# Kernel optimization log

Hardware: AMD Instinct MI355X
Metric: run time of the kernel (lower is better)

The kernel has to match this reference:

```python
import jax, jax.numpy as jnp
import numpy as np

B, N, DIM = 8, 2048, 1024
EPSILON = 0.03
SCALE = 1.0 / np.sqrt(DIM).astype(np.float32)


def setup_inputs() -> dict:
    key = jax.random.key(0)
    ks = jax.random.split(key, 5)
    Q = jax.random.normal(ks[0], (B, N, DIM), dtype=jnp.float32)
    K = jax.random.normal(ks[1], (B, N, DIM), dtype=jnp.float32)
    V = jax.random.normal(ks[2], (B, N, DIM), dtype=jnp.float32)
    # H_net: Linear(dim, dim//2) -> SiLU -> Linear(dim//2, 1); init like torch default scale-ish
    W1 = jax.random.normal(ks[3], (DIM, DIM // 2), dtype=jnp.float32) * (1.0 / np.sqrt(DIM))
    b1 = jnp.zeros((DIM // 2,), dtype=jnp.float32)
    W2 = jax.random.normal(ks[4], (DIM // 2, 1), dtype=jnp.float32) * (1.0 / np.sqrt(DIM // 2))
    b2 = jnp.zeros((1,), dtype=jnp.float32)
    return {"Q": Q, "K": K, "V": V, "W1": W1, "b1": b1, "W2": W2, "b2": b2}


def _mlp(x, W1, b1, W2, b2):
    h = jax.nn.silu(x @ W1 + b1)  # [B,N,dim//2]
    return h @ W2 + b2            # [B,N,1]


def reference(Q, K, V, W1, b1, W2, b2):
    def energy(q, v):
        # scores [B,N,N]
        A = jax.nn.softmax(jnp.einsum('bnd,bmd->bnm', q, K) * SCALE, axis=-1)
        attn_out = jnp.einsum('bnm,bmd->bnd', A, v)
        H = jnp.sum(_mlp(attn_out, W1, b1, W2, b2))
        return H, attn_out

    # grads of scalar energy H w.r.t. Q and V (dH_dV is computed per the
    # original code but discarded by the final split; only dH_dQ survives)
    (dH_dQ, dH_dV), attn_out = jax.grad(energy, argnums=(0, 1), has_aux=True)(Q, V)
    # S_new = cat([Q,V]) + eps*cat([dH_dV, -dH_dQ]); split -> V_new = V - eps*dH_dQ
    V_new = V - EPSILON * dH_dQ
    return V_new + attn_out
```

## Files before the change

### kernel.cpp

```cpp
#include <hip/hip_runtime.h>

typedef __bf16 bf16;
typedef long i64;
typedef __attribute__((ext_vector_type(8))) __bf16 bf16x8;
typedef __attribute__((ext_vector_type(4))) float f32x4;
typedef __attribute__((ext_vector_type(4))) int i32x4;

#define MEMFENCE asm volatile("" ::: "memory")

__device__ __forceinline__ unsigned char tofp8(float x) {
    return (unsigned char)(__builtin_amdgcn_cvt_pk_fp8_f32(x, x, 0, false) & 0xff);
}

__device__ __forceinline__ void gload16(const void* g, void* l) {
    __builtin_amdgcn_global_load_lds(
        (const __attribute__((address_space(1))) void*)g,
        (__attribute__((address_space(3))) void*)l,
        16, 0, 0);
}

template<int EPI, int F8>
__global__ __launch_bounds__(512, 1)
void gemm8p(const void* __restrict__ A, const void* __restrict__ Bm,
            void* __restrict__ Cp, int Kdim, int lda, int ldb, int ldc,
            long sA, long sB, long sC, float alpha,
            const float* __restrict__ aux1, const bf16* __restrict__ aux3)
{
    constexpr int ES = F8 ? 1 : 2;
    __shared__ __align__(16) char smem[163840];

    const int gx = gridDim.x, gy = gridDim.y;
    int lin = blockIdx.x + gx * (blockIdx.y + gy * blockIdx.z);
    const int q = (gx * gy * gridDim.z) >> 3;
    lin = (lin & 7) * q + (lin >> 3);
    const int bx = lin % gx;
    const int rem0 = lin / gx;
    const int by = rem0 % gy;
    const int bz = rem0 / gy;

    const int t0 = threadIdx.x;
    const int w = t0 >> 6, lane = t0 & 63;
    const int wm = w >> 2, wn = w & 3;
    const int m0 = by * 256, n0 = bx * 256;
    const long zb = bz;

    const char* Ab = (const char*)A + ((size_t)zb * sA + (size_t)m0 * lda) * ES;
    const char* Bb = (const char*)Bm + ((size_t)zb * sB + (size_t)n0 * ldb) * ES;

    const int sr16 = lane >> 2;
    const int sceB = F8 ? ((((lane & 3) ^ (sr16 & 3) ^ (((lane >> 5) & 1) << 1)) << 4))
                        : ((((lane & 3) << 4) ^ (((lane >> 5) & 1) << 5)));
    const int r0s = (w >> 1) * 16 + sr16;
    const int c0sB = (w & 1) * 64 + sceB;
    const char* gA0 = Ab + (size_t)r0s * lda * ES + c0sB;
    const char* gA1 = Ab + (size_t)(128 + r0s) * lda * ES + c0sB;
    const char* gB0 = Bb + (size_t)r0s * ldb * ES + c0sB;
    const char* gB1 = Bb + (size_t)(128 + r0s) * ldb * ES + c0sB;
    const size_t a64 = (size_t)64 * lda * ES, b64 = (size_t)64 * ldb * ES;
    const int ldsW0 = w * 1024, ldsW1 = (8 + w) * 1024;

    const int lr = lane & 15, lkq = lane >> 4;
    const int phx = ((lane >> 3) & 1) << 5;
    const int frag_base = F8 ? (lr * 64) : ((lr * 64 + lkq * 16) ^ phx);
    const int e0 = (((0 + (lkq >> 1)) ^ (lr & 3) ^ (((lr >> 3) & 1) << 1)) << 4) + ((lkq & 1) << 3);
    const int e1 = (((2 + (lkq >> 1)) ^ (lr & 3) ^ (((lr >> 3) & 1) << 1)) << 4) + ((lkq & 1) << 3);
    const char* aR = smem + wm * 16384 + frag_base;
    const char* bR = smem + 98304 + (wn >> 1) * 16384 + (wn & 1) * 8192 + frag_base;

    f32x4 acc[8][4] = {};
    const int NTt = Kdim >> (F8 ? 7 : 6);

    auto stgA = [&](int h, int u, int off) {
        char* L = smem + off + h * 16384;
        const char* g = h ? gA1 : gA0;
        gload16(g + (size_t)u * 128,        L + ldsW0);
        gload16(g + a64 + (size_t)u * 128,  L + ldsW1);
    };
    auto stgB = [&](int h, int u, int p) {
        char* L = smem + 98304 + p * 32768 + h * 16384;
        const char* g = h ? gB1 : gB0;
        gload16(g + (size_t)u * 128,        L + ldsW0);
        gload16(g + b64 + (size_t)u * 128,  L + ldsW1);
    };

    stgA(0, 0, 0);     stgA(1, 0, 0);     stgB(0, 0, 0); stgB(1, 0, 0);
    stgA(0, 1, 32768); stgA(1, 1, 32768); stgB(0, 1, 1); stgB(1, 1, 1);
    asm volatile("s_waitcnt vmcnt(8)" ::: "memory");
    __builtin_amdgcn_s_barrier();
    MEMFENCE;

    bf16x8 a[4][2], bl[2][2], bh[2][2];
    i64 a8[4][2][2], bl8[2][2][2], bh8[2][2][2];

#define RD8(DST, BASE, SUB)                                                \
    DST[0] = *(const i64*)((BASE) + (SUB) * 1024 + e0);                    \
    DST[1] = *(const i64*)((BASE) + (SUB) * 1024 + e1);

    if constexpr (!F8) {
        #pragma unroll
        for (int mf = 0; mf < 4; ++mf)
            #pragma unroll
            for (int ks = 0; ks < 2; ++ks)
                a[mf][ks] = *(const bf16x8*)(aR + (mf * 2 + ks) * 1024);
        #pragma unroll
        for (int nf = 0; nf < 2; ++nf)
            #pragma unroll
            for (int ks = 0; ks < 2; ++ks)
                bh[nf][ks] = *(const bf16x8*)(bR + ((2 + nf) * 2 + ks) * 1024);
    } else {
        #pragma unroll
        for (int mf = 0; mf < 4; ++mf)
            #pragma unroll
            for (int ks = 0; ks < 2; ++ks) { RD8(a8[mf][ks], aR, mf * 2 + ks) }
        #pragma unroll
        for (int nf = 0; nf < 2; ++nf)
            #pragma unroll
            for (int ks = 0; ks < 2; ++ks) { RD8(bh8[nf][ks], bR, (2 + nf) * 2 + ks) }
    }

#define QUADQ(MFB, NFB, AARR, BARR)                                                     \
    __builtin_amdgcn_s_setprio(1);                                                      \
    _Pragma("unroll")                                                                   \
    for (int ks = 0; ks < 2; ++ks)                                                      \
        _Pragma("unroll")                                                               \
        for (int mf = 0; mf < 4; ++mf)                                                  \
            _Pragma("unroll")                                                           \
            for (int nf = 0; nf < 2; ++nf)                                              \
                acc[(MFB) + mf][(NFB) + nf] = __builtin_amdgcn_mfma_f32_16x16x32_bf16(  \
                    AARR[mf][ks], BARR[nf][ks], acc[(MFB) + mf][(NFB) + nf], 0, 0, 0);  \
    __builtin_amdgcn_s_setprio(0);

#define QUAD8(MFB, NFB, AARR, BARR)                                                     \
    __builtin_amdgcn_s_setprio(1);                                                      \
    _Pragma("unroll")                                                                   \
    for (int ks = 0; ks < 2; ++ks)                                                      \
        _Pragma("unroll")                                                               \
        for (int k2 = 0; k2 < 2; ++k2)                                                  \
            _Pragma("unroll")                                                           \
            for (int mf = 0; mf < 4; ++mf)                                              \
                _Pragma("unroll")                                                       \
                for (int nf = 0; nf < 2; ++nf)                                          \
                    acc[(MFB) + mf][(NFB) + nf] =                                       \
                        __builtin_amdgcn_mfma_f32_16x16x32_fp8_fp8(                     \
                            AARR[mf][ks][k2], BARR[nf][ks][k2],                         \
                            acc[(MFB) + mf][(NFB) + nf], 0, 0, 0);                      \
    __builtin_amdgcn_s_setprio(0);

    int aOff = 0, aOff1 = 32768, sOff = 65536;
    for (int u = 0; u < NTt; ++u) {
        const int p = u & 1;
        const char* aP  = aR + aOff;
        const char* aP1 = aR + aOff1;
        const char* bP  = bR + p * 32768;
        const char* bP1 = bR + (p ^ 1) * 32768;
        const bool st2 = (u + 2 < NTt), nx = (u + 1 < NTt);

        if (st2) stgA(0, u + 2, sOff);
        if constexpr (!F8) {
            #pragma unroll
            for (int nf = 0; nf < 2; ++nf)
                #pragma unroll
                for (int ks = 0; ks < 2; ++ks)
                    bl[nf][ks] = *(const bf16x8*)(bP + (nf * 2 + ks) * 1024);
            QUADQ(0, 2, a, bh)
        } else {
            #pragma unroll
            for (int nf = 0; nf < 2; ++nf)
                #pragma unroll
                for (int ks = 0; ks < 2; ++ks) { RD8(bl8[nf][ks], bP, nf * 2 + ks) }
            QUAD8(0, 2, a8, bh8)
        }

        if (st2) stgA(1, u + 2, sOff);
        if constexpr (!F8) {
            QUADQ(0, 0, a, bl)
            #pragma unroll
            for (int mf = 0; mf < 4; ++mf)
                #pragma unroll
                for (int ks = 0; ks < 2; ++ks)
                    a[mf][ks] = *(const bf16x8*)(aP + ((4 + mf) * 2 + ks) * 1024);
        } else {
            QUAD8(0, 0, a8, bl8)
            #pragma unroll
            for (int mf = 0; mf < 4; ++mf)
                #pragma unroll
                for (int ks = 0; ks < 2; ++ks) { RD8(a8[mf][ks], aP, (4 + mf) * 2 + ks) }
        }
        MEMFENCE;
        if (st2)     asm volatile("s_waitcnt vmcnt(4)" ::: "memory");
        else if (nx) asm volatile("s_waitcnt vmcnt(0)" ::: "memory");
        __builtin_amdgcn_s_barrier();
        MEMFENCE;

        if (st2) stgB(0, u + 2, p);
        if constexpr (!F8) { QUADQ(4, 0, a, bl) } else { QUAD8(4, 0, a8, bl8) }

        if (st2) stgB(1, u + 2, p);
        if constexpr (!F8) {
            QUADQ(4, 2, a, bh)
            if (nx) {
                #pragma unroll
                for (int mf = 0; mf < 4; ++mf)
                    #pragma unroll
                    for (int ks = 0; ks < 2; ++ks)
                        a[mf][ks] = *(const bf16x8*)(aP1 + (mf * 2 + ks) * 1024);
                #pragma unroll
                for (int nf = 0; nf < 2; ++nf)
                    #pragma unroll
                    for (int ks = 0; ks < 2; ++ks)
                        bh[nf][ks] = *(const bf16x8*)(bP1 + ((2 + nf) * 2 + ks) * 1024);
            }
        } else {
            QUAD8(4, 2, a8, bh8)
            if (nx) {
                #pragma unroll
                for (int mf = 0; mf < 4; ++mf)
                    #pragma unroll
                    for (int ks = 0; ks < 2; ++ks) { RD8(a8[mf][ks], aP1, mf * 2 + ks) }
                #pragma unroll
                for (int nf = 0; nf < 2; ++nf)
                    #pragma unroll
                    for (int ks = 0; ks < 2; ++ks) { RD8(bh8[nf][ks], bP1, (2 + nf) * 2 + ks) }
            }
        }
        MEMFENCE;
        __builtin_amdgcn_s_barrier();
        MEMFENCE;

        const int tmp = aOff; aOff = aOff1; aOff1 = sOff; sOff = tmp;
    }
#undef QUADQ
#undef QUAD8
#undef RD8

    const int rb  = m0 + wm * 128 + lkq * 4;
    const int cb0 = n0 + wn * 64 + lr;
    #pragma unroll
    for (int mf = 0; mf < 8; ++mf) {
        #pragma unroll
        for (int r = 0; r < 4; ++r) {
            const int rw = rb + mf * 16 + r;
            float rd = 0.f;
            if (EPI == 1) {
                const size_t gr = zb * 2048 + rw;
                rd = aux1[gr] + aux1[16384 + gr] + aux1[32768 + gr] + aux1[49152 + gr];
            }
            #pragma unroll
            for (int nf = 0; nf < 4; ++nf) {
                const int c = cb0 + nf * 16;
                const size_t ix = (size_t)rw * ldc + c;
                const float v = acc[mf][nf][r];
                if (EPI == 0) {
                    ((bf16*)Cp + zb * sC)[ix] = (bf16)(alpha * v);
                } else if (EPI == 1) {
                    const bf16* Am = aux3 + zb * sC;
                    const float t = (float)Am[ix] * (v * alpha - rd) * 64.f;
                    ((unsigned char*)Cp + zb * sC)[ix] = tofp8(t);
                } else {
                    float* C = (float*)Cp + zb * sC;
                    const float* Vv = aux1 + zb * sC;
                    const bf16* AOv = aux3 + zb * sC;
                    C[ix] = Vv[ix] + (float)AOv[ix] - alpha * v;
                }
            }
        }
    }
}

template<int EPI, int NF>
__global__ __launch_bounds__(512, 1)
void gemm_nc(const bf16* __restrict__ A, const bf16* __restrict__ Bm,
             void* __restrict__ Cp, int Kdim, int lda, int ldb, int ldc,
             long sA, long sB, long sC, float alpha,
             const float* __restrict__ aux1, const float* __restrict__ aux2,
             float* __restrict__ rds)
{
    constexpr int SB = NF * 4096;
    __shared__ __align__(16) char smem[65536 + 4 * SB];

    const int gx = gridDim.x, gy = gridDim.y;
    int lin = blockIdx.x + gx * (blockIdx.y + gy * blockIdx.z);
    const int q = (gx * gy * gridDim.z) >> 3;
    lin = (lin & 7) * q + (lin >> 3);
    const int bx = lin % gx;
    const int rem0 = lin / gx;
    const int by = rem0 % gy;
    const int bz = rem0 / gy;

    const int t0 = threadIdx.x;
    const int w = t0 >> 6, lane = t0 & 63;
    const int wm = w >> 2, wn = w & 3;
    const int m0 = by * 256, n0 = bx * (64 * NF);
    const long zb = bz;

    const bf16* Ab = A  + zb * sA + (size_t)m0 * lda;
    const bf16* Bb = Bm + zb * sB + (size_t)n0 * ldb;

    const int sr16 = lane >> 2;
    const int sce  = ((((lane & 3) << 4) ^ (((lane >> 5) & 1) << 5))) >> 1;
    const int stg0 = w * 2, stg1 = w * 2 + 1;
    const bf16* pA0 = Ab + (size_t)(stg0 * 16 + sr16) * lda + sce;
    const bf16* pA1 = Ab + (size_t)(stg1 * 16 + sr16) * lda + sce;
    const bf16* pB0 = Bb + (size_t)((NF == 4 ? stg0 : w) * 16 + sr16) * ldb + sce;
    const bf16* pB1 = Bb + (size_t)(stg1 * 16 + sr16) * ldb + sce;

    const int lr = lane & 15, lkq = lane >> 4;
    const int phx = ((lane >> 3) & 1) << 5;
    const int frag_base = lr * 64 + lkq * 16;

    f32x4 acc[8][NF] = {};
    const int NT = Kdim >> 5;

    auto issueSlot = [&](int p) {
        char* lA = smem + (p & 3) * 16384;
        char* lB = smem + 65536 + (p & 3) * SB;
        const int kt = p << 5;
        gload16(pA0 + kt, lA + stg0 * 1024);
        gload16(pA1 + kt, lA + stg1 * 1024);
        if (NF == 4) {
            gload16(pB0 + kt, lB + stg0 * 1024);
            gload16(pB1 + kt, lB + stg1 * 1024);
        } else {
            gload16(pB0 + kt, lB + w * 1024);
        }
    };
    auto rdA = [&](const char* base, int sub) {
        return *(const bf16x8*)(base + (((sub << 10) + frag_base) ^ phx));
    };

    issueSlot(0); issueSlot(1); issueSlot(2);
    if (NF == 4) asm volatile("s_waitcnt vmcnt(4)" ::: "memory");
    else         asm volatile("s_waitcnt vmcnt(3)" ::: "memory");
    __builtin_amdgcn_s_barrier();
    MEMFENCE;

    bf16x8 alo[4], ahi[4], b0[NF], b1[NF];
    {
        const char* cA = smem;
        const char* cB = smem + 65536;
        #pragma unroll
        for (int mf = 0; mf < 4; ++mf) alo[mf] = rdA(cA, wm * 8 + mf);
        #pragma unroll
        for (int nf = 0; nf < NF; ++nf) b0[nf] = rdA(cB, wn * NF + nf);
    }

    auto stepBody = [&](int SL, int s, bf16x8 (&bA)[NF], bf16x8 (&bB)[NF]) {
        if (s + 3 < NT) issueSlot(s + 3);
        const char* cA = smem + SL * 16384;
        #pragma unroll
        for (int mf = 0; mf < 4; ++mf) ahi[mf] = rdA(cA, wm * 8 + 4 + mf);

        __builtin_amdgcn_s_setprio(1);
        #pragma unroll
        for (int mf = 0; mf < 4; ++mf)
            #pragma unroll
            for (int nf = 0; nf < NF; ++nf)
                acc[mf][nf] = __builtin_amdgcn_mfma_f32_16x16x32_bf16(alo[mf], bA[nf], acc[mf][nf], 0, 0, 0);
        __builtin_amdgcn_s_setprio(0);

        if (s + 1 < NT) {
            const int NS = (SL + 1) & 3;
            const char* nA = smem + NS * 16384;
            const char* nB = smem + 65536 + NS * SB;
            #pragma unroll
            for (int mf = 0; mf < 4; ++mf) alo[mf] = rdA(nA, wm * 8 + mf);
            #pragma unroll
            for (int nf = 0; nf < NF; ++nf) bB[nf] = rdA(nB, wn * NF + nf);
        }

        __builtin_amdgcn_s_setprio(1);
        #pragma unroll
        for (int mf = 0; mf < 4; ++mf)
            #pragma unroll
            for (int nf = 0; nf < NF; ++nf)
                acc[4 + mf][nf] = __builtin_amdgcn_mfma_f32_16x16x32_bf16(ahi[mf], bA[nf], acc[4 + mf][nf], 0, 0, 0);
        __builtin_amdgcn_s_setprio(0);

        MEMFENCE;
        if (s + 3 < NT) {
            if (NF == 4) asm volatile("s_waitcnt vmcnt(4)" ::: "memory");
            else         asm volatile("s_waitcnt vmcnt(3)" ::: "memory");
        } else {
            asm volatile("s_waitcnt vmcnt(0)" ::: "memory");
        }
        __builtin_amdgcn_s_barrier();
        MEMFENCE;
    };

    for (int s = 0; s < NT; s += 2) {
        stepBody(s & 3, s, b0, b1);
        stepBody((s + 1) & 3, s + 1, b1, b0);
    }

    const int rb  = m0 + wm * 128 + lkq * 4;
    const int cb0 = n0 + wn * (NF * 16) + lr;

    if (EPI == 0 || EPI == 4) {
        #pragma unroll
        for (int mf = 0; mf < 8; ++mf)
            #pragma unroll
            for (int nf = 0; nf < NF; ++nf) {
                const int c = cb0 + nf * 16;
                #pragma unroll
                for (int r = 0; r < 4; ++r) {
                    const int rw = rb + mf * 16 + r;
                    const size_t ix = (size_t)rw * ldc + c;
                    if (EPI == 0)
                        ((bf16*)Cp + zb * sC)[ix] = (bf16)(alpha * acc[mf][nf][r]);
                    else
                        ((unsigned char*)Cp + zb * sC)[ix] = tofp8(alpha * acc[mf][nf][r]);
                }
            }
    } else {
        float* smemF = (float*)smem;
        #pragma unroll
        for (int mf = 0; mf < 8; ++mf) {
            #pragma unroll
            for (int r = 0; r < 4; ++r) {
                const int rw = rb + mf * 16 + r;
                float pd = 0.f;
                #pragma unroll
                for (int nf = 0; nf < NF; ++nf) {
                    const int c = cb0 + nf * 16;
                    const float v = acc[mf][nf][r];
                    const float u = v + aux1[c];
                    const float sg = 1.f / (1.f + __expf(-u));
                    const float dd = sg * (1.f + u * (1.f - sg));
                    const float uval = dd * aux2[c];
                    ((unsigned char*)Cp)[(size_t)rw * ldc + c] = tofp8(uval * 16.f);
                    pd += uval * v;
                }
                #pragma unroll
                for (int o = 1; o < 16; o <<= 1) pd += __shfl_xor(pd, o, 64);
                if (lr == 0)
                    smemF[wn * 256 + wm * 128 + mf * 16 + lkq * 4 + r] = pd;
            }
        }
        __syncthreads();
        if (t0 < 256) {
            const float s4 = smemF[t0] + smemF[256 + t0] + smemF[512 + t0] + smemF[768 + t0];
            rds[(size_t)bx * 16384 + m0 + t0] = s4;
        }
    }
}

template<bool DN, int TM>
__device__ __forceinline__ void transcast_body(
                 const float* __restrict__ in, bf16* __restrict__ outN,
                 void* __restrict__ outT, int R, int C, int bx, int by, int bz,
                 float (*ts)[65])
{
    const int t = threadIdx.x;
    const int c0 = bx * 64, r0 = by * 64;
    const size_t zoff = (size_t)bz * R * C;

    const int rr = t >> 2, cc = (t & 3) * 16;
    float4 f[4];
    const float* src = in + zoff + (size_t)(r0 + rr) * C + c0 + cc;
    #pragma unroll
    for (int i = 0; i < 4; ++i) f[i] = *(const float4*)(src + 4 * i);

    if (DN) {
        bf16x8 h0, h1;
        #pragma unroll
        for (int i = 0; i < 2; ++i) {
            h0[i*4+0] = (bf16)f[i].x;   h0[i*4+1] = (bf16)f[i].y;
            h0[i*4+2] = (bf16)f[i].z;   h0[i*4+3] = (bf16)f[i].w;
            h1[i*4+0] = (bf16)f[i+2].x; h1[i*4+1] = (bf16)f[i+2].y;
            h1[i*4+2] = (bf16)f[i+2].z; h1[i*4+3] = (bf16)f[i+2].w;
        }
        bf16* dst = outN + zoff + (size_t)(r0 + rr) * C + c0 + cc;
        *(bf16x8*)dst = h0;
        *(bf16x8*)(dst + 8) = h1;
    }
    if (TM) {
        #pragma unroll
        for (int i = 0; i < 4; ++i) {
            ts[rr][cc + 4*i + 0] = f[i].x;
            ts[rr][cc + 4*i + 1] = f[i].y;
            ts[rr][cc + 4*i + 2] = f[i].z;
            ts[rr][cc + 4*i + 3] = f[i].w;
        }
        __syncthreads();
        const int ct = t >> 2, rr4 = (t & 3) * 16;
        if (TM == 1) {
            bf16x8 o0, o1;
            #pragma unroll
            for (int i = 0; i < 8; ++i) o0[i] = (bf16)ts[rr4 + i][ct];
            #pragma unroll
            for (int i = 0; i < 8; ++i) o1[i] = (bf16)ts[rr4 + 8 + i][ct];
            bf16* dst = (bf16*)outT + zoff + (size_t)(c0 + ct) * R + r0 + rr4;
            *(bf16x8*)dst = o0;
            *(bf16x8*)(dst + 8) = o1;
        } else {
            i32x4 o;
            #pragma unroll
            for (int g = 0; g < 4; ++g) {
                int v = __builtin_amdgcn_cvt_pk_fp8_f32(ts[rr4 + 4*g + 0][ct], ts[rr4 + 4*g + 1][ct], 0, false);
                v = __builtin_amdgcn_cvt_pk_fp8_f32(ts[rr4 + 4*g + 2][ct], ts[rr4 + 4*g + 3][ct], v, true);
                o[g] = v;
            }
            unsigned char* dst = (unsigned char*)outT + zoff + (size_t)(c0 + ct) * R + r0 + rr4;
            *(i32x4*)dst = o;
        }
    }
}

__global__ __launch_bounds__(256)
void trans_all(const float* __restrict__ Q, const float* __restrict__ Km,
               const float* __restrict__ V, const float* __restrict__ W1,
               bf16* __restrict__ Qb, bf16* __restrict__ Kb, unsigned char* __restrict__ KbT8,
               bf16* __restrict__ Vb, bf16* __restrict__ VbT, bf16* __restrict__ W1T)
{
    __shared__ float ts[64][65];
    const int z = blockIdx.z;
    if (z < 8) {
        transcast_body<true, 0>(Q, Qb, nullptr, 2048, 1024, blockIdx.x, blockIdx.y, z, ts);
    } else if (z < 16) {
        transcast_body<true, 2>(Km, Kb, KbT8, 2048, 1024, blockIdx.x, blockIdx.y, z - 8, ts);
    } else if (z < 24) {
        transcast_body<true, 1>(V, Vb, VbT, 2048, 1024, blockIdx.x, blockIdx.y, z - 16, ts);
    } else {
        if (blockIdx.x < 8 && blockIdx.y < 16)
            transcast_body<false, 1>(W1, nullptr, W1T, 1024, 512, blockIdx.x, blockIdx.y, 0, ts);
    }
}

__global__ __launch_bounds__(256)
void softmax_k(const bf16* __restrict__ S, bf16* __restrict__ A)
{
    const size_t row = blockIdx.x;
    const int t = threadIdx.x;
    const int wid = t >> 6, lane = t & 63;
    __shared__ float r1[4], r2[4];

    bf16x8 v = *(const bf16x8*)(S + row * 2048 + t * 8);
    float f[8];
    float mx = -1e30f;
    #pragma unroll
    for (int i = 0; i < 8; ++i) { f[i] = (float)v[i]; mx = fmaxf(mx, f[i]); }
    #pragma unroll
    for (int o = 32; o; o >>= 1) mx = fmaxf(mx, __shfl_xor(mx, o, 64));
    if (!lane) r1[wid] = mx;
    __syncthreads();
    mx = fmaxf(fmaxf(r1[0], r1[1]), fmaxf(r1[2], r1[3]));

    float sum = 0.f;
    #pragma unroll
    for (int i = 0; i < 8; ++i) { f[i] = __expf(f[i] - mx); sum += f[i]; }
    #pragma unroll
    for (int o = 32; o; o >>= 1) sum += __shfl_xor(sum, o, 64);
    if (!lane) r2[wid] = sum;
    __syncthreads();
    sum = r2[0] + r2[1] + r2[2] + r2[3];

    const float inv = 1.f / sum;
    bf16x8 ov;
    #pragma unroll
    for (int i = 0; i < 8; ++i) ov[i] = (bf16)(f[i] * inv);
    *(bf16x8*)(A + row * 2048 + t * 8) = ov;
}

extern "C" void kernel_launch(void* const* d_in, const int* in_sizes, int n_in,
                              void* d_out, int out_size, void* d_ws, size_t ws_size,
                              hipStream_t stream)
{
    const float* Q  = (const float*)d_in[0];
    const float* Km = (const float*)d_in[1];
    const float* V  = (const float*)d_in[2];
    const float* W1 = (const float*)d_in[3];
    const float* b1 = (const float*)d_in[4];
    const float* W2 = (const float*)d_in[5];
    float* out = (float*)d_out;

    char* ws = (char*)d_ws;
    bf16* Amat = (bf16*)(ws);
    bf16* AO   = (bf16*)(ws + 67108864);
    bf16* Kb   = AO;
    unsigned char* KbT8 = (unsigned char*)(ws + 100663296);
    float* rdSlab = (float*)(ws + 117440512);
    bf16* Vb   = (bf16*)(ws + 134217728);
    unsigned char* dS8 = (unsigned char*)(ws + 134217728);
    bf16* VbT  = (bf16*)(ws + 167772160);
    unsigned char* U8 = (unsigned char*)(ws + 167772160);
    bf16* Qb   = (bf16*)(ws + 201326592);
    unsigned char* VW18 = (unsigned char*)(ws + 201326592);
    bf16* W1T  = (bf16*)(ws + 234881024);
    bf16* S    = (bf16*)d_out;

    const long sQK = 2048L * 1024;
    const long sS  = 2048L * 2048;
    const long sVW = 2048L * 512;
    dim3 blk(256), blkG(512);

    trans_all<<<dim3(16, 32, 25), blk, 0, stream>>>(Q, Km, V, W1, Qb, Kb, KbT8, Vb, VbT, W1T);

    gemm8p<0, 0><<<dim3(8, 8, 8), blkG, 0, stream>>>(
        Qb, Kb, S, 1024, 1024, 1024, 2048, sQK, sQK, sS, 0.03125f, nullptr, nullptr);

    gemm_nc<4, 2><<<dim3(4, 8, 8), blkG, 0, stream>>>(
        Vb, W1T, VW18, 1024, 1024, 1024, 512, sQK, 0, sVW, 1.0f, nullptr, nullptr, nullptr);

    softmax_k<<<dim3(16384), blk, 0, stream>>>(S, Amat);

    gemm8p<0, 0><<<dim3(4, 8, 8), blkG, 0, stream>>>(
        Amat, VbT, AO, 2048, 2048, 2048, 1024, sS, sQK, sQK, 1.0f, nullptr, nullptr);

    gemm_nc<3, 2><<<dim3(4, 64, 1), blkG, 0, stream>>>(
        AO, W1T, U8, 1024, 1024, 1024, 512, 0, 0, 0, 1.0f, b1, W2, rdSlab);

    gemm8p<1, 1><<<dim3(8, 8, 8), blkG, 0, stream>>>(
        U8, VW18, dS8, 512, 512, 512, 2048, 1048576, 1048576, 4194304, 0.0625f, rdSlab, Amat);

    gemm8p<2, 1><<<dim3(4, 8, 8), blkG, 0, stream>>>(
        dS8, KbT8, out, 2048, 2048, 2048, 1024, 4194304, 2097152, 2097152,
        0.03f * 0.03125f / 64.f, V, AO);
}
```

Baseline: 402.5 us.

## Pre-permute FP8 operand columns so fragments load with one 16-byte LDS read

The FP8 operand producers (transpose-cast, GEMM epilogues, SiLU-derivative epilogue) now write bytes in a permuted column order given by pcol. This lets the FP8 GEMM read each fragment with a single 16-byte LDS load, where it previously did two 8-byte loads with XOR swizzle offsets, and it reuses the bf16 staging swizzle. The cost is scattered byte-granularity global stores and split 8-byte stores in the transposer, and the permutation must match the MFMA K ordering exactly.

```diff
diff --git a/kernel.cpp b/kernel.cpp
--- a/kernel.cpp
+++ b/kernel.cpp
@@ -2,6 +2,8 @@
 
 typedef __bf16 bf16;
 typedef long i64;
+typedef __attribute__((ext_vector_type(2))) long i64x2;
+typedef __attribute__((ext_vector_type(2))) int i32x2;
 typedef __attribute__((ext_vector_type(8))) __bf16 bf16x8;
 typedef __attribute__((ext_vector_type(4))) float f32x4;
 typedef __attribute__((ext_vector_type(4))) int i32x4;
@@ -10,6 +12,9 @@
 
 __device__ __forceinline__ unsigned char tofp8(float x) {
     return (unsigned char)(__builtin_amdgcn_cvt_pk_fp8_f32(x, x, 0, false) & 0xff);
+}
+__device__ __forceinline__ int pcol(int c) {
+    return (c & ~63) | (((c >> 3) & 3) << 4) | (((c >> 5) & 1) << 3) | (c & 7);
 }
 
 __device__ __forceinline__ void gload16(const void* g, void* l) {
@@ -48,8 +53,7 @@
     const char* Bb = (const char*)Bm + ((size_t)zb * sB + (size_t)n0 * ldb) * ES;
 
     const int sr16 = lane >> 2;
-    const int sceB = F8 ? ((((lane & 3) ^ (sr16 & 3) ^ (((lane >> 5) & 1) << 1)) << 4))
-                        : ((((lane & 3) << 4) ^ (((lane >> 5) & 1) << 5)));
+    const int sceB = (((lane & 3) << 4) ^ (((lane >> 5) & 1) << 5));
     const int r0s = (w >> 1) * 16 + sr16;
     const int c0sB = (w & 1) * 64 + sceB;
     const char* gA0 = Ab + (size_t)r0s * lda * ES + c0sB;
@@ -61,9 +65,7 @@
 
     const int lr = lane & 15, lkq = lane >> 4;
     const int phx = ((lane >> 3) & 1) << 5;
-    const int frag_base = F8 ? (lr * 64) : ((lr * 64 + lkq * 16) ^ phx);
-    const int e0 = (((0 + (lkq >> 1)) ^ (lr & 3) ^ (((lr >> 3) & 1) << 1)) << 4) + ((lkq & 1) << 3);
-    const int e1 = (((2 + (lkq >> 1)) ^ (lr & 3) ^ (((lr >> 3) & 1) << 1)) << 4) + ((lkq & 1) << 3);
+    const int frag_base = (lr * 64 + lkq * 16) ^ phx;
     const char* aR = smem + wm * 16384 + frag_base;
     const char* bR = smem + 98304 + (wn >> 1) * 16384 + (wn & 1) * 8192 + frag_base;
 
@@ -90,11 +92,9 @@
     MEMFENCE;
 
     bf16x8 a[4][2], bl[2][2], bh[2][2];
-    i64 a8[4][2][2], bl8[2][2][2], bh8[2][2][2];
-
-#define RD8(DST, BASE, SUB)                                                \
-    DST[0] = *(const i64*)((BASE) + (SUB) * 1024 + e0);                    \
-    DST[1] = *(const i64*)((BASE) + (SUB) * 1024 + e1);
+    i64x2 a8[4][2], bl8[2][2], bh8[2][2];
+
+#define RD8(DST, BASE, SUB)  DST = *(const i64x2*)((BASE) + (SUB) * 1024);
 
     if constexpr (!F8) {
         #pragma unroll
@@ -255,7 +255,7 @@
                 } else if (EPI == 1) {
                     const bf16* Am = aux3 + zb * sC;
                     const float t = (float)Am[ix] * (v * alpha - rd) * 64.f;
-                    ((unsigned char*)Cp + zb * sC)[ix] = tofp8(t);
+                    ((unsigned char*)Cp + zb * sC)[(size_t)rw * ldc + pcol(c)] = tofp8(t);
                 } else {
                     float* C = (float*)Cp + zb * sC;
                     const float* Vv = aux1 + zb * sC;
@@ -404,11 +404,10 @@
                 #pragma unroll
                 for (int r = 0; r < 4; ++r) {
                     const int rw = rb + mf * 16 + r;
-                    const size_t ix = (size_t)rw * ldc + c;
                     if (EPI == 0)
-                        ((bf16*)Cp + zb * sC)[ix] = (bf16)(alpha * acc[mf][nf][r]);
+                        ((bf16*)Cp + zb * sC)[(size_t)rw * ldc + c] = (bf16)(alpha * acc[mf][nf][r]);
                     else
-                        ((unsigned char*)Cp + zb * sC)[ix] = tofp8(alpha * acc[mf][nf][r]);
+                        ((unsigned char*)Cp + zb * sC)[(size_t)rw * ldc + pcol(c)] = tofp8(alpha * acc[mf][nf][r]);
                 }
             }
     } else {
@@ -427,7 +426,7 @@
                     const float sg = 1.f / (1.f + __expf(-u));
                     const float dd = sg * (1.f + u * (1.f - sg));
                     const float uval = dd * aux2[c];
-                    ((unsigned char*)Cp)[(size_t)rw * ldc + c] = tofp8(uval * 16.f);
+                    ((unsigned char*)Cp)[(size_t)rw * ldc + pcol(c)] = tofp8(uval * 16.f);
                     pd += uval * v;
                 }
                 #pragma unroll
@@ -500,8 +499,12 @@
                 v = __builtin_amdgcn_cvt_pk_fp8_f32(ts[rr4 + 4*g + 2][ct], ts[rr4 + 4*g + 3][ct], v, true);
                 o[g] = v;
             }
-            unsigned char* dst = (unsigned char*)outT + zoff + (size_t)(c0 + ct) * R + r0 + rr4;
-            *(i32x4*)dst = o;
+            const int plo = ((rr4 & 31) << 1) + ((rr4 >> 5) << 3);
+            unsigned char* dstb = (unsigned char*)outT + zoff + (size_t)(c0 + ct) * R + r0;
+            i32x2 lo; lo[0] = o[0]; lo[1] = o[1];
+            i32x2 hi; hi[0] = o[2]; hi[1] = o[3];
+            *(i32x2*)(dstb + plo) = lo;
+            *(i32x2*)(dstb + plo + 16) = hi;
         }
     }
 }
```

After: 382.7 us. 1.05x faster.
